# Performance work log

Measured on AMD Instinct MI355X. Metric: run time of the kernel, lower is better.

The kernel has to match this reference:

```python
import jax, jax.numpy as jnp
import numpy as np

K = 32          # k_value
NUM_CLASSES = 10


def setup_inputs() -> dict:
    key = jax.random.key(0)
    k1, k2, k3 = jax.random.split(key, 3)
    queries = jax.random.normal(k1, (1024, 64), dtype=jnp.float32)
    train_data = jax.random.normal(k2, (200000, 64), dtype=jnp.float32)
    train_labels = jax.random.randint(k3, (200000,), 0, NUM_CLASSES, dtype=jnp.int32)
    return {"queries": queries, "train_data": train_data, "train_labels": train_labels}


def _votes(queries, train_data, train_labels):
    # Squared Euclidean distance [Q, N] via the ||q||^2 + ||x||^2 - 2 q.x expansion
    # (same math as sum of squared differences, O(Q*N*d) without a Q*N*d temp).
    q2 = jnp.sum(queries * queries, axis=1, keepdims=True)        # [Q, 1]
    x2 = jnp.sum(train_data * train_data, axis=1)                  # [N]
    sim = q2 + x2[None, :] - 2.0 * (queries @ train_data.T)        # [Q, N]
    sim = jnp.maximum(sim, 0.0)  # exact squared distances are >= 0
    # Inversion kernel: replace exact zeros with 0.1, then weights = 1/sim.
    sim = jnp.where(sim == 0.0, jnp.float32(0.1), sim)
    weights = 1.0 / sim                                            # [Q, N]
    # Top-K weights (largest weight == nearest neighbor).
    top_w, top_i = jax.lax.top_k(weights, K)                       # [Q, K]
    top_lab = train_labels[top_i]                                  # [Q, K] int
    # segment_sum over labels == scatter-add weights per class.
    Q = queries.shape[0]
    rows = jnp.arange(Q)[:, None]                                  # [Q, 1]
    votes = jnp.zeros((Q, NUM_CLASSES), dtype=top_w.dtype).at[rows, top_lab].add(top_w)
    return votes


def reference(queries, train_data, train_labels):
    votes = _votes(queries, train_data, train_labels)
    # argmax over class weight sums == tf.argmax(segment_sum) per query
    return jnp.argmax(votes, axis=1)
```

## Files before the change

### kernel.cpp

```cpp
#include <hip/hip_runtime.h>
#include <hip/hip_bf16.h>
#include <hip/hip_fp16.h>

#define N_TRAIN 200000
#define DIMS    64
#define NQ      1024
#define KSEL    32
#define NCLS    10

#define CHROWS2 391
#define NBLK0   512
#define LCAP    8
#define OVFCAP  256
#define TOTC    4096
#define MAXS    1536
#define SAMPLES 8192
#define SROWS   32
#define NPB     3125

typedef float f32x4 __attribute__((ext_vector_type(4)));
typedef short f16x8 __attribute__((ext_vector_type(8)));

__device__ __forceinline__ unsigned fmap(float f) {
    unsigned u = __float_as_uint(f);
    return u ^ ((u >> 31) ? 0xFFFFFFFFu : 0x80000000u);
}
__device__ __forceinline__ float funmap(unsigned m) {
    unsigned u = m ^ ((m >> 31) ? 0x80000000u : 0xFFFFFFFFu);
    return __uint_as_float(u);
}
__device__ __forceinline__ unsigned short f2h(float f) {
    union { __half h; unsigned short u; } c;
    c.h = __float2half_rn(f);
    return c.u;
}
__device__ __forceinline__ f16x8 pack8h(float4 a, float4 b) {
    f16x8 r;
    r[0] = (short)f2h(a.x); r[1] = (short)f2h(a.y);
    r[2] = (short)f2h(a.z); r[3] = (short)f2h(a.w);
    r[4] = (short)f2h(b.x); r[5] = (short)f2h(b.y);
    r[6] = (short)f2h(b.z); r[7] = (short)f2h(b.w);
    return r;
}

__global__ __launch_bounds__(512) void k_prep(const float* __restrict__ X,
                                              float* __restrict__ x2,
                                              float* __restrict__ bmax,
                                              short* __restrict__ Xh) {
    int T = blockIdx.x * 512 + threadIdx.x;
    int row = T >> 3;
    int l8 = T & 7;
    const float4* xp = (const float4*)(X + (long)row * 64 + l8 * 8);
    float4 a = xp[0], b = xp[1];
    *(f16x8*)(Xh + (long)row * 64 + l8 * 8) = pack8h(a, b);
    float p = a.x * a.x + a.y * a.y + a.z * a.z + a.w * a.w +
              b.x * b.x + b.y * b.y + b.z * b.z + b.w * b.w;
    p += __shfl_xor(p, 1);
    p += __shfl_xor(p, 2);
    p += __shfl_xor(p, 4);
    if (l8 == 0) x2[row] = p;
    float m = p;
    m = fmaxf(m, __shfl_xor(m, 8));
    m = fmaxf(m, __shfl_xor(m, 16));
    m = fmaxf(m, __shfl_xor(m, 32));
    __shared__ float wm[8];
    if ((threadIdx.x & 63) == 0) wm[threadIdx.x >> 6] = m;
    __syncthreads();
    if (threadIdx.x == 0) {
        float r = wm[0];
#pragma unroll
        for (int i = 1; i < 8; i++) r = fmaxf(r, wm[i]);
        bmax[blockIdx.x] = r;
    }
}

__global__ __launch_bounds__(256) void k_max(const float* __restrict__ bmax,
                                             float* __restrict__ x2maxf) {
    float m = -1e30f;
    for (int i = threadIdx.x; i < NPB; i += 256) m = fmaxf(m, bmax[i]);
#pragma unroll
    for (int d = 1; d < 64; d <<= 1) m = fmaxf(m, __shfl_xor(m, d));
    __shared__ float wm[4];
    if ((threadIdx.x & 63) == 0) wm[threadIdx.x >> 6] = m;
    __syncthreads();
    if (threadIdx.x == 0)
        *x2maxf = fmaxf(fmaxf(wm[0], wm[1]), fmaxf(wm[2], wm[3]));
}

__global__ __launch_bounds__(256) void k_cvt(const float* __restrict__ src,
                                             short* __restrict__ dst) {
    long c = (long)blockIdx.x * 256 + threadIdx.x;
    const float4* xp = (const float4*)(src + c * 8);
    float4 a = xp[0], b = xp[1];
    *(f16x8*)(dst + c * 8) = pack8h(a, b);
}

template<int MODE>
__global__ __launch_bounds__(512) void k_dist(
    const short* __restrict__ Xh, const short* __restrict__ Qh,
    const float* __restrict__ x2, const float* __restrict__ tqw,
    unsigned* __restrict__ pcnt, unsigned* __restrict__ pool,
    unsigned* __restrict__ ovfcnt, uint2* __restrict__ ovf,
    unsigned short* __restrict__ keys) {
    int bid = blockIdx.x;
    int tid = threadIdx.x;
    int qt = tid >> 6;
    int lane = tid & 63;
    int lr = lane & 15;
    int lk = lane >> 4;

    __shared__ unsigned lcnt[MODE == 0 ? NQ : 1];
    __shared__ unsigned lbuf[MODE == 0 ? NQ * LCAP : 1];

    int r0 = MODE ? (bid * SROWS) : bid * CHROWS2;
    int rowEnd = MODE ? (r0 + SROWS) : min(r0 + CHROWS2, N_TRAIN);

    if (MODE == 0) {
        lcnt[tid] = 0u;
        lcnt[tid + 512] = 0u;
        __syncthreads();
    }

    f16x8 afr[8][2];
#pragma unroll
    for (int qi = 0; qi < 8; qi++) {
        const short* qp = Qh + (long)((qt << 7) + (qi << 4) + lr) * 64 + (lk << 3);
        afr[qi][0] = *(const f16x8*)qp;
        afr[qi][1] = *(const f16x8*)(qp + 32);
    }
    float htq[8];
    if (MODE == 0) {
#pragma unroll
        for (int qi = 0; qi < 8; qi++) {
            float4 t4 = *(const float4*)(tqw + (qt << 7) + (qi << 4) + (lk << 2));
            htq[qi] = 0.5f * fmaxf(fmaxf(t4.x, t4.y), fmaxf(t4.z, t4.w));
        }
    }

    for (int base = r0; base < rowEnd; base += 16) {
        int row = base + lr;
        bool valid = row < rowEnd;
        int rowc = valid ? row : (rowEnd - 1);
        const short* xp = Xh + (long)rowc * 64 + (lk << 3);
        f16x8 b0 = *(const f16x8*)xp;
        f16x8 b1 = *(const f16x8*)(xp + 32);
        float x2c = valid ? x2[rowc] : 1e30f;
        float hx = 0.5f * x2c;

#pragma unroll
        for (int qi = 0; qi < 8; qi++) {
            f32x4 acc = {0.f, 0.f, 0.f, 0.f};
            acc = __builtin_amdgcn_mfma_f32_16x16x32_f16(afr[qi][0], b0, acc, 0, 0, 0);
            acc = __builtin_amdgcn_mfma_f32_16x16x32_f16(afr[qi][1], b1, acc, 0, 0, 0);
            if (MODE == 1) {
#pragma unroll
                for (int r4 = 0; r4 < 4; r4++) {
                    unsigned k16 = fmap(x2c - 2.f * acc[r4]) >> 16;
                    unsigned o = (unsigned)__shfl_xor((int)k16, 1);
                    unsigned v2 = k16 | (o << 16);
                    unsigned p2 = (unsigned)__shfl_xor((int)v2, 2);
                    if ((lr & 3) == 0) {
                        int qg = (qt << 7) + (qi << 4) + (lk << 2) + r4;
                        *(uint2*)(&keys[(long)qg * SAMPLES + row]) = make_uint2(v2, p2);
                    }
                }
            } else {
                float mx = fmaxf(fmaxf(acc[0], acc[1]), fmaxf(acc[2], acc[3]));
                if (valid && mx + htq[qi] >= hx) {
                    float4 t4 = *(const float4*)(tqw + (qt << 7) + (qi << 4) + (lk << 2));
                    float tq4[4] = {t4.x, t4.y, t4.z, t4.w};
#pragma unroll
                    for (int r4 = 0; r4 < 4; r4++) {
                        if (acc[r4] + 0.5f * tq4[r4] >= hx) {
                            int qg = (qt << 7) + (qi << 4) + (lk << 2) + r4;
                            unsigned entry = (fmap(x2c - 2.f * acc[r4]) & 0xFFFFFE00u) |
                                             (unsigned)(row - r0);
                            unsigned slot = atomicAdd(&lcnt[qg], 1u);
                            if (slot < LCAP) {
                                lbuf[qg * LCAP + slot] = entry;
                            } else {
                                unsigned o = atomicAdd(&ovfcnt[qg], 1u);
                                if (o < OVFCAP)
                                    ovf[qg * OVFCAP + o] =
                                        make_uint2(entry >> 9, (unsigned)row);
                            }
                        }
                    }
                }
            }
        }
    }

    if (MODE == 0) {
        __syncthreads();
        for (int q = tid; q < NQ; q += 512) {
            unsigned lc = min(lcnt[q], (unsigned)LCAP);
            pcnt[(bid << 10) + q] = lc;
            uint4 a = *(uint4*)&lbuf[q * LCAP];
            uint4 b = *(uint4*)&lbuf[q * LCAP + 4];
            long base = ((long)(bid << 10) + q) * LCAP;
            *(uint4*)&pool[base] = a;
            *(uint4*)&pool[base + 4] = b;
        }
    }
}

__global__ __launch_bounds__(256) void k_sel(const unsigned short* __restrict__ keys,
                                             const float* __restrict__ Qm,
                                             const float* __restrict__ x2maxf,
                                             float* __restrict__ tqw,
                                             float* __restrict__ q2g) {
    int q = blockIdx.x, tid = threadIdx.x;
    unsigned short mk[32];
#pragma unroll
    for (int m = 0; m < 32; m++) mk[m] = keys[(long)q * SAMPLES + tid + 256 * m];
    __shared__ float q2s_;
    __shared__ int cnt;
    if (tid < 64) {
        float v = Qm[(long)q * 64 + tid];
        float p = v * v;
#pragma unroll
        for (int d = 1; d < 64; d <<= 1) p += __shfl_xor(p, d);
        if (tid == 0) q2s_ = p;
    }
    unsigned lo = 0, hi = 65535;
    for (int it = 0; it < 16; ++it) {
        __syncthreads();
        if (tid == 0) cnt = 0;
        __syncthreads();
        unsigned mid = (lo + hi) >> 1;
        int c = 0;
#pragma unroll
        for (int m = 0; m < 32; m++) c += (mk[m] <= mid) ? 1 : 0;
#pragma unroll
        for (int d = 1; d < 64; d <<= 1) c += __shfl_xor(c, d);
        if ((tid & 63) == 0) atomicAdd(&cnt, c);
        __syncthreads();
        if (cnt >= KSEL) hi = mid; else lo = mid + 1;
    }
    if (tid == 0) {
        unsigned vv = hi + 2u; if (vv > 65535u) vv = 65535u;
        float t = funmap(vv << 16);
        float q2 = q2s_;
        tqw[q] = t + 0.004f * sqrtf(q2 * (*x2maxf)) + 0.1f;
        q2g[q] = q2;
    }
}

__global__ __launch_bounds__(256) void k_merge(const float* __restrict__ Qm,
                                               const float* __restrict__ X,
                                               const float* __restrict__ x2,
                                               const int* __restrict__ labels,
                                               const unsigned* __restrict__ pcnt,
                                               const unsigned* __restrict__ pool,
                                               const unsigned* __restrict__ ovfcnt,
                                               const uint2* __restrict__ ovf,
                                               const float* __restrict__ q2g,
                                               const float* __restrict__ x2maxf,
                                               int* __restrict__ out) {
    int q = blockIdx.x, tid = threadIdx.x;
    __shared__ unsigned eK[TOTC];
    __shared__ int eR[TOTC];
    __shared__ int sR[MAXS];
    __shared__ float sKey[MAXS];
    __shared__ int sLab[MAXS];
    __shared__ float qs[64];
    __shared__ int tot, cnt, ns, nw, nt;
    __shared__ unsigned cutS;
    __shared__ float wKey[34];
    __shared__ int wLab[34];
    __shared__ int tIdx[64];
    __shared__ int tLab[64];

    if (tid == 0) { tot = 0; ns = 0; nw = 0; nt = 0; }
    if (tid < 64) qs[tid] = Qm[(long)q * 64 + tid];
    __syncthreads();

    for (int b = tid; b < NBLK0; b += 256) {
        unsigned lc = pcnt[(b << 10) + q];
        if (lc) {
            long base = ((long)(b << 10) + q) * LCAP;
            uint4 a = *(const uint4*)&pool[base];
            uint4 bb = *(const uint4*)&pool[base + 4];
            int p = atomicAdd(&tot, (int)lc);
            int rbase = b * CHROWS2;
#pragma unroll
            for (int i = 0; i < LCAP; i++) {
                unsigned e = (i == 0) ? a.x : (i == 1) ? a.y : (i == 2) ? a.z :
                             (i == 3) ? a.w : (i == 4) ? bb.x : (i == 5) ? bb.y :
                             (i == 6) ? bb.z : bb.w;
                int p2 = p + i;
                if ((unsigned)i < lc && p2 < TOTC) {
                    eK[p2] = e >> 9;
                    eR[p2] = rbase + (int)(e & 511u);
                }
            }
        }
    }
    int ov = min((int)ovfcnt[q], OVFCAP);
    for (int i = tid; i < ov; i += 256) {
        uint2 e = ovf[q * OVFCAP + i];
        int p = atomicAdd(&tot, 1);
        if (p < TOTC) { eK[p] = e.x; eR[p] = (int)e.y; }
    }
    __syncthreads();
    int T = min(tot, TOTC);

    unsigned mk[16];
#pragma unroll
    for (int m = 0; m < 16; m++) { int i = tid + (m << 8); mk[m] = (i < T) ? eK[i] : 0xFFFFFFFFu; }
    unsigned lo = 0, hi = 0x7FFFFFu;
    for (int it = 0; it < 23; ++it) {
        __syncthreads();
        if (tid == 0) cnt = 0;
        __syncthreads();
        unsigned mid = (lo + hi) >> 1;
        int c = 0;
#pragma unroll
        for (int m = 0; m < 16; m++) c += (mk[m] <= mid) ? 1 : 0;
#pragma unroll
        for (int d = 1; d < 64; d <<= 1) c += __shfl_xor(c, d);
        if ((tid & 63) == 0) atomicAdd(&cnt, c);
        __syncthreads();
        if (cnt >= KSEL) hi = mid; else lo = mid + 1;
    }
    float q2v = q2g[q];
    if (tid == 0) {
        unsigned vv = min(hi + 1u, 0x7FFFFFu);
        float tf = funmap(vv << 9);
        float err = 0.004f * sqrtf(q2v * (*x2maxf)) + 0.1f;
        cutS = min((fmap(tf + err) >> 9) + 1u, 0x7FFFFFu);
    }
    __syncthreads();
    unsigned cut = cutS;
    for (int i = tid; i < T; i += 256)
        if (eK[i] <= cut) { int p = atomicAdd(&ns, 1); if (p < MAXS) sR[p] = eR[i]; }
    __syncthreads();
    int NS = min(ns, MAXS);

    for (int i = tid; i < NS; i += 256) {
        int row = sR[i];
        const float4* xr = (const float4*)(X + (long)row * 64);
        const float4* qr = (const float4*)qs;
        float dot = 0.f;
#pragma unroll
        for (int k4 = 0; k4 < 16; k4++) {
            float4 xv = xr[k4], qv = qr[k4];
            dot += qv.x * xv.x + qv.y * xv.y + qv.z * xv.z + qv.w * xv.w;
        }
        sKey[i] = x2[row] - 2.f * dot;
        sLab[i] = labels[row];
    }
    __syncthreads();

    unsigned uk[6];
#pragma unroll
    for (int m = 0; m < 6; m++) { int i = tid + (m << 8); uk[m] = (i < NS) ? fmap(sKey[i]) : 0xFFFFFFFFu; }
    unsigned lo2 = 0u, hi2 = 0xFFFFFFFFu;
    for (int it = 0; it < 32; ++it) {
        __syncthreads();
        if (tid == 0) cnt = 0;
        __syncthreads();
        unsigned mid = lo2 + ((hi2 - lo2) >> 1);
        int c = 0;
#pragma unroll
        for (int m = 0; m < 6; m++) c += (uk[m] <= mid) ? 1 : 0;
#pragma unroll
        for (int d = 1; d < 64; d <<= 1) c += __shfl_xor(c, d);
        if ((tid & 63) == 0) atomicAdd(&cnt, c);
        __syncthreads();
        if (cnt >= KSEL) hi2 = mid; else lo2 = mid + 1;
    }
    unsigned T32 = hi2;

#pragma unroll
    for (int m = 0; m < 6; m++) {
        int i = tid + (m << 8);
        if (i < NS) {
            if (uk[m] < T32) {
                int p = atomicAdd(&nw, 1);
                if (p < 34) { wKey[p] = sKey[i]; wLab[p] = sLab[i]; }
            } else if (uk[m] == T32) {
                int p = atomicAdd(&nt, 1);
                if (p < 64) { tIdx[p] = sR[i]; tLab[p] = sLab[i]; }
            }
        }
    }
    __syncthreads();

    if (tid == 0) {
        float votes[NCLS] = {0.f, 0.f, 0.f, 0.f, 0.f, 0.f, 0.f, 0.f, 0.f, 0.f};
        int NW = min(nw, 32);
        for (int i = 0; i < NW; i++) {
            float dist = q2v + wKey[i];
            if (dist < 0.f) dist = 0.f;
            if (dist == 0.f) dist = 0.1f;
            votes[wLab[i]] += 1.f / dist;
        }
        int need = KSEL - NW;
        int NT = min(nt, 64);
        float tkey = funmap(T32);
        float dist = q2v + tkey;
        if (dist < 0.f) dist = 0.f;
        if (dist == 0.f) dist = 0.1f;
        float twgt = 1.f / dist;
        for (int t = 0; t < need && t < NT; t++) {
            int best = -1, bi = 0x7FFFFFFF;
            for (int u = 0; u < NT; u++)
                if (tIdx[u] < bi) { bi = tIdx[u]; best = u; }
            if (best < 0) break;
            votes[tLab[best]] += twgt;
            tIdx[best] = 0x7FFFFFFF;
        }
        float bv = votes[0];
        int bc = 0;
#pragma unroll
        for (int c = 1; c < NCLS; c++)
            if (votes[c] > bv) { bv = votes[c]; bc = c; }
        out[q] = bc;
    }
}

extern "C" void kernel_launch(void* const* d_in, const int* in_sizes, int n_in,
                              void* d_out, int out_size, void* d_ws, size_t ws_size,
                              hipStream_t stream) {
    const float* Qm = (const float*)d_in[0];
    const float* X = (const float*)d_in[1];
    const int* labels = (const int*)d_in[2];
    char* ws = (char*)d_ws;
    float* x2 = (float*)(ws + 0);
    float* tqw = (float*)(ws + 800000);
    float* q2g = (float*)(ws + 804096);
    float* x2maxf = (float*)(ws + 808192);
    float* bmax = (float*)(ws + 808256);
    unsigned* pcnt = (unsigned*)(ws + 820800);
    unsigned* ovfcnt = (unsigned*)(ws + 2917952);
    uint2* ovf = (uint2*)(ws + 2922048);
    unsigned short* keys = (unsigned short*)(ws + 5019200);
    unsigned* pool = (unsigned*)(ws + 5019200);
    short* Xh = (short*)(ws + 21796416);
    short* Qh = (short*)(ws + 47396416);
    int* out = (int*)d_out;

    hipMemsetAsync(ovfcnt, 0, 4096, stream);
    k_prep<<<NPB, 512, 0, stream>>>(X, x2, bmax, Xh);
    k_max<<<1, 256, 0, stream>>>(bmax, x2maxf);
    k_cvt<<<32, 256, 0, stream>>>(Qm, Qh);
    k_dist<1><<<SAMPLES / SROWS, 512, 0, stream>>>(Xh, Qh, x2, tqw, pcnt, pool, ovfcnt, ovf, keys);
    k_sel<<<NQ, 256, 0, stream>>>(keys, Qm, x2maxf, tqw, q2g);
    k_dist<0><<<NBLK0, 512, 0, stream>>>(Xh, Qh, x2, tqw, pcnt, pool, ovfcnt, ovf, keys);
    k_merge<<<NQ, 256, 0, stream>>>(Qm, X, x2, labels, pcnt, pool, ovfcnt, ovf, q2g, x2maxf, out);
}
```

Baseline: 244.6 us.

## Split distance blocks across query halves and prefetch next training tile

Result: no change. 249.0 us (+1.8%).

```diff
diff --git a/kernel.cpp b/kernel.cpp
--- a/kernel.cpp
+++ b/kernel.cpp
@@ -9,7 +9,8 @@
 #define NCLS    10
 
 #define CHROWS2 391
-#define NBLK0   512
+#define NCHUNK  512
+#define NBLK0   1024
 #define LCAP    8
 #define OVFCAP  256
 #define TOTC    4096
@@ -104,51 +105,69 @@
     unsigned short* __restrict__ keys) {
     int bid = blockIdx.x;
     int tid = threadIdx.x;
-    int qt = tid >> 6;
+    int qh = bid & 1;
+    int cb = bid >> 1;
+    int w = tid >> 6;
     int lane = tid & 63;
     int lr = lane & 15;
     int lk = lane >> 4;
 
-    __shared__ unsigned lcnt[MODE == 0 ? NQ : 1];
-    __shared__ unsigned lbuf[MODE == 0 ? NQ * LCAP : 1];
-
-    int r0 = MODE ? (bid * SROWS) : bid * CHROWS2;
+    __shared__ unsigned lcnt[MODE == 0 ? 512 : 1];
+    __shared__ unsigned lbuf[MODE == 0 ? 512 * LCAP : 1];
+
+    int r0 = MODE ? cb * SROWS : cb * CHROWS2;
     int rowEnd = MODE ? (r0 + SROWS) : min(r0 + CHROWS2, N_TRAIN);
 
     if (MODE == 0) {
         lcnt[tid] = 0u;
-        lcnt[tid + 512] = 0u;
-        __syncthreads();
-    }
-
-    f16x8 afr[8][2];
-#pragma unroll
-    for (int qi = 0; qi < 8; qi++) {
-        const short* qp = Qh + (long)((qt << 7) + (qi << 4) + lr) * 64 + (lk << 3);
+        __syncthreads();
+    }
+
+    int qbase = (qh << 9) + (w << 6);
+
+    f16x8 afr[4][2];
+#pragma unroll
+    for (int qi = 0; qi < 4; qi++) {
+        const short* qp = Qh + (long)(qbase + (qi << 4) + lr) * 64 + (lk << 3);
         afr[qi][0] = *(const f16x8*)qp;
         afr[qi][1] = *(const f16x8*)(qp + 32);
     }
-    float htq[8];
+    float htq[4];
     if (MODE == 0) {
 #pragma unroll
-        for (int qi = 0; qi < 8; qi++) {
-            float4 t4 = *(const float4*)(tqw + (qt << 7) + (qi << 4) + (lk << 2));
+        for (int qi = 0; qi < 4; qi++) {
+            float4 t4 = *(const float4*)(tqw + qbase + (qi << 4) + (lk << 2));
             htq[qi] = 0.5f * fmaxf(fmaxf(t4.x, t4.y), fmaxf(t4.z, t4.w));
         }
     }
 
+    f16x8 cb0, cb1;
+    float cx2;
+    {
+        int rowc = min(r0 + lr, rowEnd - 1);
+        const short* xp = Xh + (long)rowc * 64 + (lk << 3);
+        cb0 = *(const f16x8*)xp;
+        cb1 = *(const f16x8*)(xp + 32);
+        cx2 = (r0 + lr < rowEnd) ? x2[rowc] : 1e30f;
+    }
+
     for (int base = r0; base < rowEnd; base += 16) {
+        f16x8 b0 = cb0, b1 = cb1;
+        float x2c = cx2;
+        int nb = base + 16;
+        if (nb < rowEnd) {
+            int rowc = min(nb + lr, rowEnd - 1);
+            const short* xp = Xh + (long)rowc * 64 + (lk << 3);
+            cb0 = *(const f16x8*)xp;
+            cb1 = *(const f16x8*)(xp + 32);
+            cx2 = (nb + lr < rowEnd) ? x2[rowc] : 1e30f;
+        }
         int row = base + lr;
         bool valid = row < rowEnd;
-        int rowc = valid ? row : (rowEnd - 1);
-        const short* xp = Xh + (long)rowc * 64 + (lk << 3);
-        f16x8 b0 = *(const f16x8*)xp;
-        f16x8 b1 = *(const f16x8*)(xp + 32);
-        float x2c = valid ? x2[rowc] : 1e30f;
         float hx = 0.5f * x2c;
 
 #pragma unroll
-        for (int qi = 0; qi < 8; qi++) {
+        for (int qi = 0; qi < 4; qi++) {
             f32x4 acc = {0.f, 0.f, 0.f, 0.f};
             acc = __builtin_amdgcn_mfma_f32_16x16x32_f16(afr[qi][0], b0, acc, 0, 0, 0);
             acc = __builtin_amdgcn_mfma_f32_16x16x32_f16(afr[qi][1], b1, acc, 0, 0, 0);
@@ -160,24 +179,25 @@
                     unsigned v2 = k16 | (o << 16);
                     unsigned p2 = (unsigned)__shfl_xor((int)v2, 2);
                     if ((lr & 3) == 0) {
-                        int qg = (qt << 7) + (qi << 4) + (lk << 2) + r4;
+                        int qg = qbase + (qi << 4) + (lk << 2) + r4;
                         *(uint2*)(&keys[(long)qg * SAMPLES + row]) = make_uint2(v2, p2);
                     }
                 }
             } else {
                 float mx = fmaxf(fmaxf(acc[0], acc[1]), fmaxf(acc[2], acc[3]));
                 if (valid && mx + htq[qi] >= hx) {
-                    float4 t4 = *(const float4*)(tqw + (qt << 7) + (qi << 4) + (lk << 2));
+                    float4 t4 = *(const float4*)(tqw + qbase + (qi << 4) + (lk << 2));
                     float tq4[4] = {t4.x, t4.y, t4.z, t4.w};
 #pragma unroll
                     for (int r4 = 0; r4 < 4; r4++) {
                         if (acc[r4] + 0.5f * tq4[r4] >= hx) {
-                            int qg = (qt << 7) + (qi << 4) + (lk << 2) + r4;
+                            int qg = qbase + (qi << 4) + (lk << 2) + r4;
+                            int ql = qg & 511;
                             unsigned entry = (fmap(x2c - 2.f * acc[r4]) & 0xFFFFFE00u) |
                                              (unsigned)(row - r0);
-                            unsigned slot = atomicAdd(&lcnt[qg], 1u);
+                            unsigned slot = atomicAdd(&lcnt[ql], 1u);
                             if (slot < LCAP) {
-                                lbuf[qg * LCAP + slot] = entry;
+                                lbuf[ql * LCAP + slot] = entry;
                             } else {
                                 unsigned o = atomicAdd(&ovfcnt[qg], 1u);
                                 if (o < OVFCAP)
@@ -193,15 +213,14 @@
 
     if (MODE == 0) {
         __syncthreads();
-        for (int q = tid; q < NQ; q += 512) {
-            unsigned lc = min(lcnt[q], (unsigned)LCAP);
-            pcnt[(bid << 10) + q] = lc;
-            uint4 a = *(uint4*)&lbuf[q * LCAP];
-            uint4 b = *(uint4*)&lbuf[q * LCAP + 4];
-            long base = ((long)(bid << 10) + q) * LCAP;
-            *(uint4*)&pool[base] = a;
-            *(uint4*)&pool[base + 4] = b;
-        }
+        int ql = tid;
+        unsigned lc = min(lcnt[ql], (unsigned)LCAP);
+        pcnt[((long)bid << 9) + ql] = lc;
+        uint4 a = *(uint4*)&lbuf[ql * LCAP];
+        uint4 b = *(uint4*)&lbuf[ql * LCAP + 4];
+        long base = (((long)bid << 9) + ql) * LCAP;
+        *(uint4*)&pool[base] = a;
+        *(uint4*)&pool[base + 4] = b;
     }
 }
 
@@ -276,14 +295,16 @@
     if (tid < 64) qs[tid] = Qm[(long)q * 64 + tid];
     __syncthreads();
 
-    for (int b = tid; b < NBLK0; b += 256) {
-        unsigned lc = pcnt[(b << 10) + q];
+    int qh = q >> 9, ql = q & 511;
+    for (int c2 = tid; c2 < NCHUNK; c2 += 256) {
+        int b = (c2 << 1) | qh;
+        unsigned lc = pcnt[((long)b << 9) + ql];
         if (lc) {
-            long base = ((long)(b << 10) + q) * LCAP;
+            long base = (((long)b << 9) + ql) * LCAP;
             uint4 a = *(const uint4*)&pool[base];
             uint4 bb = *(const uint4*)&pool[base + 4];
             int p = atomicAdd(&tot, (int)lc);
-            int rbase = b * CHROWS2;
+            int rbase = c2 * CHROWS2;
 #pragma unroll
             for (int i = 0; i < LCAP; i++) {
                 unsigned e = (i == 0) ? a.x : (i == 1) ? a.y : (i == 2) ? a.z :
@@ -446,7 +467,7 @@
     k_prep<<<NPB, 512, 0, stream>>>(X, x2, bmax, Xh);
     k_max<<<1, 256, 0, stream>>>(bmax, x2maxf);
     k_cvt<<<32, 256, 0, stream>>>(Qm, Qh);
-    k_dist<1><<<SAMPLES / SROWS, 512, 0, stream>>>(Xh, Qh, x2, tqw, pcnt, pool, ovfcnt, ovf, keys);
+    k_dist<1><<<2 * (SAMPLES / SROWS), 512, 0, stream>>>(Xh, Qh, x2, tqw, pcnt, pool, ovfcnt, ovf, keys);
     k_sel<<<NQ, 256, 0, stream>>>(keys, Qm, x2maxf, tqw, q2g);
     k_dist<0><<<NBLK0, 512, 0, stream>>>(Xh, Qh, x2, tqw, pcnt, pool, ovfcnt, ovf, keys);
     k_merge<<<NQ, 256, 0, stream>>>(Qm, X, x2, labels, pcnt, pool, ovfcnt, ovf, q2g, x2maxf, out);
```
